# Optimization experiments

Hardware: AMD Instinct MI355X
Metric: run time of the kernel (lower is better)

Reference implementation:

```python
import jax, jax.numpy as jnp
import numpy as np

RMS_EPS = 1e-6
B, S, H = 2, 4096, 4096
N_Q_OUT, N_KV_OUT = 4096, 1024  # 32 heads * 128, 8 kv heads * 128


def setup_inputs() -> dict:
    key = jax.random.key(0)
    k1, k2, k3, k4 = jax.random.split(key, 4)
    scale = 1.0 / np.sqrt(H)
    return {
        "hidden_states": jax.random.normal(k1, (B, S, H), dtype=jnp.float32),
        "gamma": jnp.ones((H,), dtype=jnp.float32),
        "w_q": jax.random.normal(k2, (H, N_Q_OUT), dtype=jnp.float32) * scale,
        "w_k": jax.random.normal(k3, (H, N_KV_OUT), dtype=jnp.float32) * scale,
        "w_v": jax.random.normal(k4, (H, N_KV_OUT), dtype=jnp.float32) * scale,
    }


def _rmsnorm(x, gamma, eps=RMS_EPS):
    # x: [B, S, H]; normalize over last axis
    var = jnp.mean(jnp.square(x), axis=-1, keepdims=True)
    return x * jax.lax.rsqrt(var + eps) * gamma


def reference(hidden_states, gamma, w_q, w_k, w_v):
    # Fused RMSNorm + QKV projection (GQA): normalize once, then three
    # column-parallel matmuls sharing the normalized activation.
    xn = _rmsnorm(hidden_states, gamma)  # [B, S, H]
    q = jnp.einsum("bsh,hd->bsd", xn, w_q)  # [B, S, n_heads*head_dim]
    k = jnp.einsum("bsh,hd->bsd", xn, w_k)  # [B, S, n_kv_heads*head_dim]
    v = jnp.einsum("bsh,hd->bsd", xn, w_v)  # [B, S, n_kv_heads*head_dim]
    return q, k, v
```

## Files before the change

kernel.cpp:

```cpp
#include <hip/hip_runtime.h>
#include <hip/hip_bf16.h>
#include <stdint.h>

#define HD      4096
#define MROWS   8192
#define NQ      4096
#define NKV     1024
#define NTOT    6144
#define RMS_EPS 1e-6f

typedef __attribute__((ext_vector_type(8))) short bf16x8;
typedef __attribute__((ext_vector_type(16))) float f32x16;

static __device__ __forceinline__ unsigned short f2bf(float f) {
  union { float f; unsigned u; } a; a.f = f;
  unsigned r = a.u + 0x7FFFu + ((a.u >> 16) & 1u);
  return (unsigned short)(r >> 16);
}

__global__ __launch_bounds__(256) void prep_kernel(
    const float* __restrict__ x, const float* __restrict__ gamma,
    const float* __restrict__ wq, const float* __restrict__ wk,
    const float* __restrict__ wv,
    unsigned short* __restrict__ xn, unsigned short* __restrict__ wt) {
  __shared__ float smem[32 * 33];
  const int bid = blockIdx.x;
  const int t = threadIdx.x;
  if (bid < MROWS) {
    const float4* xr = (const float4*)(x + (size_t)bid * HD);
    const float4* g4 = (const float4*)gamma;
    float4 v[4];
    float ss = 0.f;
#pragma unroll
    for (int i = 0; i < 4; ++i) {
      v[i] = xr[t + i * 256];
      ss += v[i].x * v[i].x + v[i].y * v[i].y + v[i].z * v[i].z + v[i].w * v[i].w;
    }
#pragma unroll
    for (int o = 32; o > 0; o >>= 1) ss += __shfl_xor(ss, o, 64);
    if ((t & 63) == 0) smem[t >> 6] = ss;
    __syncthreads();
    const float tot = smem[0] + smem[1] + smem[2] + smem[3];
    const float rstd = rsqrtf(tot * (1.f / HD) + RMS_EPS);
    ushort4* xo = (ushort4*)(xn + (size_t)bid * HD);
#pragma unroll
    for (int i = 0; i < 4; ++i) {
      const float4 g = g4[t + i * 256];
      ushort4 o;
      o.x = f2bf(v[i].x * rstd * g.x);
      o.y = f2bf(v[i].y * rstd * g.y);
      o.z = f2bf(v[i].z * rstd * g.z);
      o.w = f2bf(v[i].w * rstd * g.w);
      xo[t + i * 256] = o;
    }
  } else {
    int b2 = bid - MROWS;
    const float* w; unsigned short* dst; int Nw, nb, kt;
    if (b2 < 16384)      { w = wq; dst = wt;                           Nw = NQ;  nb = b2 & 127; kt = b2 >> 7; }
    else if (b2 < 20480) { b2 -= 16384; w = wk; dst = wt + (size_t)NQ * HD;         Nw = NKV; nb = b2 & 31; kt = b2 >> 5; }
    else                 { b2 -= 20480; w = wv; dst = wt + (size_t)(NQ + NKV) * HD; Nw = NKV; nb = b2 & 31; kt = b2 >> 5; }
    const int r = t >> 3, c4 = t & 7;
    const float4 vin = *(const float4*)&w[(size_t)(kt * 32 + r) * Nw + nb * 32 + c4 * 4];
    smem[r * 33 + c4 * 4 + 0] = vin.x;
    smem[r * 33 + c4 * 4 + 1] = vin.y;
    smem[r * 33 + c4 * 4 + 2] = vin.z;
    smem[r * 33 + c4 * 4 + 3] = vin.w;
    __syncthreads();
    ushort4 o;
    o.x = f2bf(smem[(c4 * 4 + 0) * 33 + r]);
    o.y = f2bf(smem[(c4 * 4 + 1) * 33 + r]);
    o.z = f2bf(smem[(c4 * 4 + 2) * 33 + r]);
    o.w = f2bf(smem[(c4 * 4 + 3) * 33 + r]);
    *(ushort4*)&dst[(size_t)(nb * 32 + r) * HD + kt * 32 + c4 * 4] = o;
  }
}


static __device__ __forceinline__ void gload_lds16(const unsigned short* g,
                                                   unsigned short* l) {
  __builtin_amdgcn_global_load_lds(
      (const __attribute__((address_space(1))) void*)g,
      (__attribute__((address_space(3))) void*)l, 16, 0, 0);
}

#define VM4 asm volatile("s_waitcnt vmcnt(4)" ::: "memory")
#define VM0 asm volatile("s_waitcnt vmcnt(0)" ::: "memory")
#define BAR __builtin_amdgcn_s_barrier()

#define RDA(AK, QM)                                                            \
  do {                                                                         \
    _Pragma("unroll") for (int mi = 0; mi < 2; ++mi)                           \
      _Pragma("unroll") for (int ks = 0; ks < 4; ++ks)                         \
        ar[mi][ks] = *(const bf16x8*)(AK[ks] + (QM) * 8192 + mi * 4096);       \
  } while (0)

#define RDB(DST, BK, QN)                                                       \
  do {                                                                         \
    _Pragma("unroll") for (int ks = 0; ks < 4; ++ks)                           \
      DST[ks] = *(const bf16x8*)(BK[ks] + (QN) * 4096);                        \
  } while (0)

#define MMA8(QM, QN, BR)                                                       \
  do {                                                                         \
    __builtin_amdgcn_s_setprio(1);                                             \
    _Pragma("unroll") for (int ks = 0; ks < 4; ++ks)                           \
      _Pragma("unroll") for (int mi = 0; mi < 2; ++mi)                         \
        acc[(QM) * 2 + mi][QN] = __builtin_amdgcn_mfma_f32_32x32x16_bf16(      \
            ar[mi][ks], BR[ks], acc[(QM) * 2 + mi][QN], 0, 0, 0);              \
    __builtin_amdgcn_s_setprio(0);                                             \
  } while (0)

__global__ __launch_bounds__(512, 2) void gemm_qkv_kernel(
    const unsigned short* __restrict__ A,
    const unsigned short* __restrict__ Bt,
    float* __restrict__ out) {
  __shared__ unsigned short lds[2][2][2][8192] __attribute__((aligned(16)));

  const int bid = blockIdx.x;
  const int xcd = bid & 7;
  const int idx = bid >> 3;
  const int sr  = idx >> 5;
  const int i32 = idx & 31;
  const int mt  = (xcd >> 1) * 8 + (i32 >> 2);
  const int nt  = (xcd & 1) * 12 + sr * 4 + (i32 & 3);
  const int m0 = mt * 256, n0 = nt * 256;

  const int tid = threadIdx.x;
  const int w = tid >> 6, lane = tid & 63;
  const int wr = w >> 2, wc = w & 3;
  const int r32 = lane & 31, hi = lane >> 5;
  const int swx = (r32 >> 1) & 7;

  const int rowoff = r32 * 128;
  const char* a0k[4]; const char* a1k[4];
  const char* b0k[4]; const char* b1k[4];
#pragma unroll
  for (int ks = 0; ks < 4; ++ks) {
    const int sl = (((ks * 2 + hi) ^ swx) << 4);
    a0k[ks] = (const char*)&lds[0][0][wr][0] + rowoff + sl;
    a1k[ks] = (const char*)&lds[0][1][wr][0] + rowoff + sl;
    b0k[ks] = (const char*)&lds[1][0][wc >> 1][0] + (wc & 1) * 8192 + rowoff + sl;
    b1k[ks] = (const char*)&lds[1][1][wc >> 1][0] + (wc & 1) * 8192 + rowoff + sl;
  }

  const int wslot = w * 512;
  const int r3 = tid >> 3;
  const unsigned scol = (unsigned)(((tid & 7) ^ ((r3 >> 1) & 7)) << 3);
  const unsigned so0 = (unsigned)r3 * HD + scol;
  const unsigned so1 = so0 + 64u * HD;

  const unsigned short* const Ab0 = A + (size_t)m0 * HD;
  const unsigned short* const Ab1 = Ab0 + (size_t)128 * HD;
  const unsigned short* const Bb0 = Bt + (size_t)n0 * HD;
  const unsigned short* const Bb1 = Bb0 + (size_t)128 * HD;

  auto STG = [&](const unsigned short* g, unsigned short* l) {
    gload_lds16(g + so0, l + wslot);
    gload_lds16(g + so1, l + 4096 + wslot);
  };

  f32x16 acc[4][2];
#pragma unroll
  for (int i = 0; i < 4; ++i)
#pragma unroll
    for (int j = 0; j < 2; ++j) acc[i][j] = (f32x16)(0.f);

  bf16x8 ar[2][4];
  bf16x8 br0[4], br1[4];

  STG(Bb0,      &lds[1][0][0][0]);
  STG(Bb1,      &lds[1][0][1][0]);
  STG(Ab0,      &lds[0][0][0][0]);
  STG(Ab1,      &lds[0][0][1][0]);
  STG(Bb0 + 64, &lds[1][1][0][0]);
  STG(Bb1 + 64, &lds[1][1][1][0]);
  VM4;
  BAR;

  for (int t = 0; t < 32; ++t) {
    const int kcs = (2 * t + 1) * 64;
    const int t2 = 2 * t + 2, t3 = 2 * t + 3;
    const int kc0 = (t2 < 64 ? t2 : 63) * 64;
    const int kc1 = (t3 < 64 ? t3 : 63) * 64;
    RDA(a0k, 0); RDB(br0, b0k, 0); STG(Ab0 + kcs, &lds[0][1][0][0]);
    BAR; MMA8(0, 0, br0); BAR;
    RDB(br1, b0k, 1);              STG(Ab1 + kcs, &lds[0][1][1][0]);
    BAR; MMA8(0, 1, br1); BAR;
    RDA(a0k, 1);                   STG(Bb0 + kc0, &lds[1][0][0][0]);
    BAR; MMA8(1, 0, br0); BAR;
                                   STG(Bb1 + kc0, &lds[1][0][1][0]); VM4;
    BAR; MMA8(1, 1, br1); BAR;
    RDA(a1k, 0); RDB(br0, b1k, 0); STG(Ab0 + kc0, &lds[0][0][0][0]);
    BAR; MMA8(0, 0, br0); BAR;
    RDB(br1, b1k, 1);              STG(Ab1 + kc0, &lds[0][0][1][0]);
    BAR; MMA8(0, 1, br1); BAR;
    RDA(a1k, 1);                   STG(Bb0 + kc1, &lds[1][1][0][0]);
    BAR; MMA8(1, 0, br0); BAR;
                                   STG(Bb1 + kc1, &lds[1][1][1][0]); VM4;
    BAR; MMA8(1, 1, br1); BAR;
  }
  VM0;

  size_t obase; int ldc, nc;
  if (n0 < NQ)            { obase = 0;                                        ldc = NQ;  nc = n0; }
  else if (n0 < NQ + NKV) { obase = (size_t)MROWS * NQ;                       ldc = NKV; nc = n0 - NQ; }
  else                    { obase = (size_t)MROWS * NQ + (size_t)MROWS * NKV; ldc = NKV; nc = n0 - NQ - NKV; }

#pragma unroll
  for (int I = 0; I < 4; ++I) {
    const int rbase = m0 + wr * 128 + I * 32 + hi * 4;
#pragma unroll
    for (int J = 0; J < 2; ++J) {
      const int col = nc + wc * 64 + J * 32 + r32;
#pragma unroll
      for (int reg = 0; reg < 16; ++reg) {
        const int row = rbase + (reg & 3) + 8 * (reg >> 2);
        out[obase + (size_t)row * ldc + col] = acc[I][J][reg];
      }
    }
  }
}

extern "C" void kernel_launch(void* const* d_in, const int* in_sizes, int n_in,
                              void* d_out, int out_size, void* d_ws, size_t ws_size,
                              hipStream_t stream) {
  const float* x     = (const float*)d_in[0];
  const float* gamma = (const float*)d_in[1];
  const float* wq    = (const float*)d_in[2];
  const float* wk    = (const float*)d_in[3];
  const float* wv    = (const float*)d_in[4];
  float* out = (float*)d_out;

  unsigned short* xn = (unsigned short*)d_ws;
  unsigned short* wt = xn + (size_t)MROWS * HD;

  prep_kernel<<<32768, 256, 0, stream>>>(x, gamma, wq, wk, wv, xn, wt);
  gemm_qkv_kernel<<<(MROWS / 256) * (NTOT / 256), 512, 0, stream>>>(xn, wt, out);
}
```

Before: 422.3 us.

## Restructure GEMM to 4-wave 128x128 warp tiles with k-sliced LDS pipeline

The QKV GEMM block moves from 8 waves to 4 waves, so each wave now computes a 128x128 output tile with 16 accumulators instead of 8. The LDS layout becomes k-slices of 16 columns with a new XOR swizzle, plus a deeper multi-stage global-to-LDS prefetch gated by vmcnt(20). The main loop is software-pipelined, interleaving register double-buffered fragment reads with MFMAs and using one barrier per step instead of two. The aim is more MFMA work per LDS read and fewer barriers. In exchange, register pressure rises sharply (256 accumulator floats per lane) and occupancy drops to one block per CU.

Measured after the change: 529.3 us. +25.3%, slower.

```diff
diff --git a/kernel.cpp b/kernel.cpp
--- a/kernel.cpp
+++ b/kernel.cpp
@@ -83,38 +83,54 @@
       (__attribute__((address_space(3))) void*)l, 16, 0, 0);
 }
 
-#define VM4 asm volatile("s_waitcnt vmcnt(4)" ::: "memory")
-#define VM0 asm volatile("s_waitcnt vmcnt(0)" ::: "memory")
-#define BAR __builtin_amdgcn_s_barrier()
-
-#define RDA(AK, QM)                                                            \
-  do {                                                                         \
-    _Pragma("unroll") for (int mi = 0; mi < 2; ++mi)                           \
-      _Pragma("unroll") for (int ks = 0; ks < 4; ++ks)                         \
-        ar[mi][ks] = *(const bf16x8*)(AK[ks] + (QM) * 8192 + mi * 4096);       \
-  } while (0)
-
-#define RDB(DST, BK, QN)                                                       \
-  do {                                                                         \
-    _Pragma("unroll") for (int ks = 0; ks < 4; ++ks)                           \
-      DST[ks] = *(const bf16x8*)(BK[ks] + (QN) * 4096);                        \
-  } while (0)
-
-#define MMA8(QM, QN, BR)                                                       \
-  do {                                                                         \
-    __builtin_amdgcn_s_setprio(1);                                             \
-    _Pragma("unroll") for (int ks = 0; ks < 4; ++ks)                           \
-      _Pragma("unroll") for (int mi = 0; mi < 2; ++mi)                         \
-        acc[(QM) * 2 + mi][QN] = __builtin_amdgcn_mfma_f32_32x32x16_bf16(      \
-            ar[mi][ks], BR[ks], acc[(QM) * 2 + mi][QN], 0, 0, 0);              \
-    __builtin_amdgcn_s_setprio(0);                                             \
-  } while (0)
-
-__global__ __launch_bounds__(512, 2) void gemm_qkv_kernel(
+#define VM20 asm volatile("s_waitcnt vmcnt(20)" ::: "memory")
+#define VM0  asm volatile("s_waitcnt vmcnt(0)" ::: "memory")
+#define BARR __builtin_amdgcn_s_barrier()
+
+#define RD(AN, BN, BUF, KS)                                                    \
+  do {                                                                         \
+    _Pragma("unroll") for (int mi = 0; mi < 4; ++mi)                           \
+      AN[mi] = *(const bf16x8*)(ab[BUF][KS] + mi * 1024);                      \
+    _Pragma("unroll") for (int j = 0; j < 4; ++j)                              \
+      BN[j] = *(const bf16x8*)(bb2[BUF][KS] + j * 1024);                       \
+  } while (0)
+
+#define MMA(AN, BN)                                                            \
+  do {                                                                         \
+    _Pragma("unroll") for (int mi = 0; mi < 4; ++mi)                           \
+      _Pragma("unroll") for (int j = 0; j < 4; ++j)                            \
+        acc[mi][j] = __builtin_amdgcn_mfma_f32_32x32x16_bf16(                  \
+            AN[mi], BN[j], acc[mi][j], 0, 0, 0);                               \
+  } while (0)
+
+#define STGA(BUF, C, KOFF)                                                     \
+  do {                                                                         \
+    gload_lds16(Ab + so0 + (KOFF), &lds[0][BUF][C][0] + w * 512);              \
+    gload_lds16(Ab + so1 + (KOFF), &lds[0][BUF][C][0] + 2048 + w * 512);       \
+  } while (0)
+#define STGB(BUF, C, KOFF)                                                     \
+  do {                                                                         \
+    gload_lds16(Bb + so0 + (KOFF), &lds[1][BUF][C][0] + w * 512);              \
+    gload_lds16(Bb + so1 + (KOFF), &lds[1][BUF][C][0] + 2048 + w * 512);       \
+  } while (0)
+
+#define TILE(B, NB, KO1, KO2)                                                  \
+  do {                                                                         \
+    RD(s1a, s1b, B, 1); STGA(NB, 3, (KO1) + 48); STGB(NB, 3, (KO1) + 48);      \
+    MMA(s0a, s0b); VM20; BARR;                                                 \
+    RD(s0a, s0b, B, 2); STGA(B, 0, (KO2));      STGB(B, 0, (KO2));             \
+    MMA(s1a, s1b); VM20; BARR;                                                 \
+    RD(s1a, s1b, B, 3); STGA(B, 1, (KO2) + 16); STGB(B, 1, (KO2) + 16);        \
+    MMA(s0a, s0b); VM20; BARR;                                                 \
+    RD(s0a, s0b, NB, 0); STGA(B, 2, (KO2) + 32); STGB(B, 2, (KO2) + 32);       \
+    MMA(s1a, s1b); VM20; BARR;                                                 \
+  } while (0)
+
+__global__ __launch_bounds__(256, 1) void gemm_qkv_kernel(
     const unsigned short* __restrict__ A,
     const unsigned short* __restrict__ Bt,
     float* __restrict__ out) {
-  __shared__ unsigned short lds[2][2][2][8192] __attribute__((aligned(16)));
+  __shared__ unsigned short lds[2][2][4][4096] __attribute__((aligned(16)));
 
   const int bid = blockIdx.x;
   const int xcd = bid & 7;
@@ -127,77 +143,54 @@
 
   const int tid = threadIdx.x;
   const int w = tid >> 6, lane = tid & 63;
-  const int wr = w >> 2, wc = w & 3;
+  const int wr = w >> 1, wc = w & 1;
   const int r32 = lane & 31, hi = lane >> 5;
-  const int swx = (r32 >> 1) & 7;
-
-  const int rowoff = r32 * 128;
-  const char* a0k[4]; const char* a1k[4];
-  const char* b0k[4]; const char* b1k[4];
-#pragma unroll
-  for (int ks = 0; ks < 4; ++ks) {
-    const int sl = (((ks * 2 + hi) ^ swx) << 4);
-    a0k[ks] = (const char*)&lds[0][0][wr][0] + rowoff + sl;
-    a1k[ks] = (const char*)&lds[0][1][wr][0] + rowoff + sl;
-    b0k[ks] = (const char*)&lds[1][0][wc >> 1][0] + (wc & 1) * 8192 + rowoff + sl;
-    b1k[ks] = (const char*)&lds[1][1][wc >> 1][0] + (wc & 1) * 8192 + rowoff + sl;
-  }
-
-  const int wslot = w * 512;
-  const int r3 = tid >> 3;
-  const unsigned scol = (unsigned)(((tid & 7) ^ ((r3 >> 1) & 7)) << 3);
-  const unsigned so0 = (unsigned)r3 * HD + scol;
-  const unsigned so1 = so0 + 64u * HD;
-
-  const unsigned short* const Ab0 = A + (size_t)m0 * HD;
-  const unsigned short* const Ab1 = Ab0 + (size_t)128 * HD;
-  const unsigned short* const Bb0 = Bt + (size_t)n0 * HD;
-  const unsigned short* const Bb1 = Bb0 + (size_t)128 * HD;
-
-  auto STG = [&](const unsigned short* g, unsigned short* l) {
-    gload_lds16(g + so0, l + wslot);
-    gload_lds16(g + so1, l + 4096 + wslot);
-  };
-
-  f32x16 acc[4][2];
+  const int swz = ((r32 >> 2) & 7) << 4;
+
+  const char* ab[2][4]; const char* bb2[2][4];
+#pragma unroll
+  for (int buf = 0; buf < 2; ++buf)
+#pragma unroll
+    for (int ks = 0; ks < 4; ++ks) {
+      ab[buf][ks]  = (const char*)&lds[0][buf][ks][0] +
+                     ((((wr * 128 + r32) * 32 + hi * 16)) ^ swz);
+      bb2[buf][ks] = (const char*)&lds[1][buf][ks][0] +
+                     ((((wc * 128 + r32) * 32 + hi * 16)) ^ swz);
+    }
+
+  const int sr0 = ((lane >> 1) ^ (lane >> 4)) & 1;
+  const int sr1 = ((lane >> 2) ^ (lane >> 5)) & 1;
+  const int shi = (lane ^ (lane >> 3)) & 1;
+  const int srow = sr0 + 2 * sr1 + 4 * ((lane >> 3) & 7) + 32 * w;
+  const unsigned so0 = (unsigned)srow * HD + shi * 8;
+  const unsigned so1 = so0 + 128u * HD;
+
+  const unsigned short* const Ab = A + (size_t)m0 * HD;
+  const unsigned short* const Bb = Bt + (size_t)n0 * HD;
+
+  f32x16 acc[4][4];
 #pragma unroll
   for (int i = 0; i < 4; ++i)
 #pragma unroll
-    for (int j = 0; j < 2; ++j) acc[i][j] = (f32x16)(0.f);
-
-  bf16x8 ar[2][4];
-  bf16x8 br0[4], br1[4];
-
-  STG(Bb0,      &lds[1][0][0][0]);
-  STG(Bb1,      &lds[1][0][1][0]);
-  STG(Ab0,      &lds[0][0][0][0]);
-  STG(Ab1,      &lds[0][0][1][0]);
-  STG(Bb0 + 64, &lds[1][1][0][0]);
-  STG(Bb1 + 64, &lds[1][1][1][0]);
-  VM4;
-  BAR;
+    for (int j = 0; j < 4; ++j) acc[i][j] = (f32x16)(0.f);
+
+  bf16x8 s0a[4], s0b[4], s1a[4], s1b[4];
+
+#pragma unroll
+  for (int c = 0; c < 4; ++c) { STGA(0, c, c * 16); STGB(0, c, c * 16); }
+#pragma unroll
+  for (int c = 0; c < 3; ++c) { STGA(1, c, 64 + c * 16); STGB(1, c, 64 + c * 16); }
+  VM20;
+  BARR;
+  RD(s0a, s0b, 0, 0);
 
   for (int t = 0; t < 32; ++t) {
-    const int kcs = (2 * t + 1) * 64;
-    const int t2 = 2 * t + 2, t3 = 2 * t + 3;
-    const int kc0 = (t2 < 64 ? t2 : 63) * 64;
-    const int kc1 = (t3 < 64 ? t3 : 63) * 64;
-    RDA(a0k, 0); RDB(br0, b0k, 0); STG(Ab0 + kcs, &lds[0][1][0][0]);
-    BAR; MMA8(0, 0, br0); BAR;
-    RDB(br1, b0k, 1);              STG(Ab1 + kcs, &lds[0][1][1][0]);
-    BAR; MMA8(0, 1, br1); BAR;
-    RDA(a0k, 1);                   STG(Bb0 + kc0, &lds[1][0][0][0]);
-    BAR; MMA8(1, 0, br0); BAR;
-                                   STG(Bb1 + kc0, &lds[1][0][1][0]); VM4;
-    BAR; MMA8(1, 1, br1); BAR;
-    RDA(a1k, 0); RDB(br0, b1k, 0); STG(Ab0 + kc0, &lds[0][0][0][0]);
-    BAR; MMA8(0, 0, br0); BAR;
-    RDB(br1, b1k, 1);              STG(Ab1 + kc0, &lds[0][0][1][0]);
-    BAR; MMA8(0, 1, br1); BAR;
-    RDA(a1k, 1);                   STG(Bb0 + kc1, &lds[1][1][0][0]);
-    BAR; MMA8(1, 0, br0); BAR;
-                                   STG(Bb1 + kc1, &lds[1][1][1][0]); VM4;
-    BAR; MMA8(1, 1, br1); BAR;
+    const int u1 = 2 * t + 1, u2 = 2 * t + 2, u3 = 2 * t + 3;
+    const int ko1 = (u1 < 64 ? u1 : 63) * 64;
+    const int ko2 = (u2 < 64 ? u2 : 63) * 64;
+    const int ko3 = (u3 < 64 ? u3 : 63) * 64;
+    TILE(0, 1, ko1, ko2);
+    TILE(1, 0, ko2, ko3);
   }
   VM0;
 
@@ -207,15 +200,15 @@
   else                    { obase = (size_t)MROWS * NQ + (size_t)MROWS * NKV; ldc = NKV; nc = n0 - NQ - NKV; }
 
 #pragma unroll
-  for (int I = 0; I < 4; ++I) {
-    const int rbase = m0 + wr * 128 + I * 32 + hi * 4;
-#pragma unroll
-    for (int J = 0; J < 2; ++J) {
-      const int col = nc + wc * 64 + J * 32 + r32;
+  for (int mi = 0; mi < 4; ++mi) {
+    const int rbase = m0 + wr * 128 + mi * 32 + hi * 4;
+#pragma unroll
+    for (int j = 0; j < 4; ++j) {
+      const int col = nc + wc * 128 + j * 32 + r32;
 #pragma unroll
       for (int reg = 0; reg < 16; ++reg) {
         const int row = rbase + (reg & 3) + 8 * (reg >> 2);
-        out[obase + (size_t)row * ldc + col] = acc[I][J][reg];
+        out[obase + (size_t)row * ldc + col] = acc[mi][j][reg];
       }
     }
   }
@@ -235,5 +228,5 @@
   unsigned short* wt = xn + (size_t)MROWS * HD;
 
   prep_kernel<<<32768, 256, 0, stream>>>(x, gamma, wq, wk, wv, xn, wt);
-  gemm_qkv_kernel<<<(MROWS / 256) * (NTOT / 256), 512, 0, stream>>>(xn, wt, out);
-}
+  gemm_qkv_kernel<<<(MROWS / 256) * (NTOT / 256), 256, 0, stream>>>(xn, wt, out);
+}
```
